# Kernel tuning notes

Hardware: AMD Instinct MI355X
Metric: run time of the kernel (lower is better)

The kernel has to match this reference:

```python
import jax, jax.numpy as jnp
import numpy as np

N_NODES = 100000
N_EDGES = 1600000
F_IN = 128
F_OUT = 64


def setup_inputs() -> dict:
    key = jax.random.key(0)
    kx, kw, kv, ks, kd = jax.random.split(key, 5)
    x = jax.random.normal(kx, (N_NODES, F_IN), dtype=jnp.float32)
    # xavier_uniform init for weight [in, out]
    limit = float(np.sqrt(6.0 / (F_IN + F_OUT)))
    weight = jax.random.uniform(kw, (F_IN, F_OUT), dtype=jnp.float32,
                                minval=-limit, maxval=limit)
    edge_val = jax.random.uniform(kv, (N_EDGES,), dtype=jnp.float32)
    edge_src = jax.random.randint(ks, (N_EDGES,), 0, N_NODES, dtype=jnp.int64)
    edge_dst = jax.random.randint(kd, (N_EDGES,), 0, N_NODES, dtype=jnp.int64)
    return {"x": x, "weight": weight, "edge_val": edge_val,
            "edge_src": edge_src, "edge_dst": edge_dst}


def reference(x, weight, edge_val, edge_src, edge_dst):
    # dropout p = 0.0 -> identity
    support = x @ weight                                  # [N, F_OUT] dense GEMM
    # spmm: out[dst] += val * support[src]  (adj row = dst, col = src)
    messages = support[edge_src] * edge_val[:, None]       # [E, F_OUT] gather
    out = jax.ops.segment_sum(messages, edge_dst,
                              num_segments=x.shape[0])     # [N, F_OUT] scatter-add
    return jax.nn.relu(out)
```

## Files before the change

### kernel.cpp

```cpp
#include <hip/hip_runtime.h>

#define F_IN 128
#define F_OUT 64
#define ROWS_PER_BLOCK 64
#define XSTRIDE 33

#define NPB 128
#define NPB_SHIFT 7
#define BCAP 800
#define ECAP 2560
#define TILE 8192
#define BSTH 1024
#define TMAX 256

__device__ inline unsigned short f2bf(float f) {
    const unsigned u = __float_as_uint(f);
    return (unsigned short)((u + 0x7FFFu + ((u >> 16) & 1u)) >> 16);
}

__global__ __launch_bounds__(512) void gemm_kernel(const float* __restrict__ x,
                                                   const float* __restrict__ w,
                                                   unsigned short* __restrict__ support,
                                                   int n_nodes) {
    __shared__ float4 w_lds[F_IN * F_OUT / 4];
    __shared__ float4 x_lds[ROWS_PER_BLOCK * XSTRIDE];

    const int tid = threadIdx.x;

    {
        const float4* w4 = (const float4*)w;
        #pragma unroll
        for (int i = tid; i < F_IN * F_OUT / 4; i += 512) w_lds[i] = w4[i];
    }

    const int row0 = blockIdx.x * ROWS_PER_BLOCK;
    {
        const float4* x4 = (const float4*)x;
        #pragma unroll
        for (int i = tid; i < ROWS_PER_BLOCK * (F_IN / 4); i += 512) {
            const int r  = i >> 5;
            const int k4 = i & 31;
            const int row = row0 + r;
            float4 v = make_float4(0.f, 0.f, 0.f, 0.f);
            if (row < n_nodes) v = x4[(size_t)row * (F_IN / 4) + k4];
            x_lds[r * XSTRIDE + k4] = v;
        }
    }
    __syncthreads();

    const int tf = tid & 15;
    const int tr = tid >> 4;
    const float* xs = (const float*)x_lds;

    float acc[2][4] = {};
    #pragma unroll 4
    for (int k = 0; k < F_IN; ++k) {
        const float4 wv = w_lds[k * 16 + tf];
        const float x0 = xs[tr * (XSTRIDE * 4) + k];
        const float x1 = xs[(tr + 32) * (XSTRIDE * 4) + k];
        acc[0][0] += x0 * wv.x; acc[0][1] += x0 * wv.y; acc[0][2] += x0 * wv.z; acc[0][3] += x0 * wv.w;
        acc[1][0] += x1 * wv.x; acc[1][1] += x1 * wv.y; acc[1][2] += x1 * wv.z; acc[1][3] += x1 * wv.w;
    }

    #pragma unroll
    for (int i = 0; i < 2; ++i) {
        const int row = row0 + tr + 32 * i;
        if (row < n_nodes) {
            ushort4 o;
            o.x = f2bf(acc[i][0]); o.y = f2bf(acc[i][1]);
            o.z = f2bf(acc[i][2]); o.w = f2bf(acc[i][3]);
            *(ushort4*)&support[(size_t)row * F_OUT + 4 * tf] = o;
        }
    }
}

__global__ __launch_bounds__(BSTH) void bscatter_kernel(const float* __restrict__ edge_val,
                                                        const int* __restrict__ edge_src,
                                                        const int* __restrict__ edge_dst,
                                                        int* __restrict__ toff,
                                                        int2* __restrict__ sorted,
                                                        int n_edges, int nb) {
    __shared__ int2 ebuf[TILE];
    __shared__ unsigned short bkt[TILE];
    __shared__ unsigned short order[TILE];
    __shared__ int h[BCAP];
    __shared__ int lcur[BCAP];
    __shared__ int wsum[16];
    __shared__ int woff_s[16];

    const int tid = threadIdx.x;
    const int te  = blockIdx.x * TILE;
    const int cnt = min(TILE, n_edges - te);

    for (int i = tid; i < BCAP; i += BSTH) h[i] = 0;
    __syncthreads();

    const int cnt4 = cnt >> 2;
    const int4*   s4 = (const int4*)(edge_src + te);
    const int4*   d4 = (const int4*)(edge_dst + te);
    const float4* v4 = (const float4*)(edge_val + te);
    for (int t = tid; t < cnt4; t += BSTH) {
        const int4   s = s4[t];
        const int4   d = d4[t];
        const float4 v = v4[t];
        const int i = t << 2;
        int b;
        b = d.x >> NPB_SHIFT; bkt[i + 0] = (unsigned short)b; atomicAdd(&h[b], 1);
        ebuf[i + 0] = make_int2(s.x | ((d.x & (NPB - 1)) << 20), __float_as_int(v.x));
        b = d.y >> NPB_SHIFT; bkt[i + 1] = (unsigned short)b; atomicAdd(&h[b], 1);
        ebuf[i + 1] = make_int2(s.y | ((d.y & (NPB - 1)) << 20), __float_as_int(v.y));
        b = d.z >> NPB_SHIFT; bkt[i + 2] = (unsigned short)b; atomicAdd(&h[b], 1);
        ebuf[i + 2] = make_int2(s.z | ((d.z & (NPB - 1)) << 20), __float_as_int(v.z));
        b = d.w >> NPB_SHIFT; bkt[i + 3] = (unsigned short)b; atomicAdd(&h[b], 1);
        ebuf[i + 3] = make_int2(s.w | ((d.w & (NPB - 1)) << 20), __float_as_int(v.w));
    }
    for (int e = (cnt4 << 2) + tid; e < cnt; e += BSTH) {
        const int dd = edge_dst[te + e];
        const int b = dd >> NPB_SHIFT;
        bkt[e] = (unsigned short)b;
        atomicAdd(&h[b], 1);
        ebuf[e] = make_int2(edge_src[te + e] | ((dd & (NPB - 1)) << 20),
                            __float_as_int(edge_val[te + e]));
    }
    __syncthreads();

    const int v = (tid < nb) ? h[tid] : 0;
    int s = v;
    #pragma unroll
    for (int off = 1; off < 64; off <<= 1) {
        const int t = __shfl_up(s, off, 64);
        if ((tid & 63) >= off) s += t;
    }
    const int wave = tid >> 6;
    if ((tid & 63) == 63) wsum[wave] = s;
    __syncthreads();
    if (tid < 16) {
        const int ws = wsum[tid];
        int sc = ws;
        #pragma unroll
        for (int off = 1; off < 16; off <<= 1) {
            const int t = __shfl_up(sc, off, 64);
            if (tid >= off) sc += t;
        }
        woff_s[tid] = sc - ws;
    }
    __syncthreads();

    int* trow = toff + (size_t)blockIdx.x * (nb + 1);
    if (tid < nb) {
        const int start = s + woff_s[wave] - v;
        lcur[tid] = start;
        trow[tid] = start;
    }
    if (tid == 0) trow[nb] = cnt;
    __syncthreads();

    for (int i = tid; i < cnt; i += BSTH) {
        const int r = atomicAdd(&lcur[bkt[i]], 1);
        order[r] = (unsigned short)i;
    }
    __syncthreads();
    for (int k = tid; k < cnt; k += BSTH)
        sorted[(size_t)te + k] = ebuf[order[k]];
}

__global__ __launch_bounds__(512) void baccum_kernel(const unsigned short* __restrict__ support,
                                                     const int2* __restrict__ sorted,
                                                     const int* __restrict__ toff,
                                                     float* __restrict__ out,
                                                     int n_nodes, int T, int nb) {
    __shared__ int2 ebuf[ECAP];
    __shared__ int2 ebuf2[ECAP];
    __shared__ int tstart[TMAX];
    __shared__ int toffb[TMAX];
    __shared__ int wsum3[4];
    __shared__ int total_s;
    __shared__ int hist[NPB];
    __shared__ int node_off[NPB + 1];
    __shared__ int cursor[NPB];
    __shared__ int wsum2[2];

    const int tid = threadIdx.x;
    const int b = blockIdx.x;

    int mycnt = 0, myoff = 0;
    if (tid < TMAX) {
        if (tid < T) {
            const int s0 = toff[(size_t)tid * (nb + 1) + b];
            const int e0 = toff[(size_t)tid * (nb + 1) + b + 1];
            toffb[tid] = s0;
            mycnt = e0 - s0;
        }
        int s = mycnt;
        #pragma unroll
        for (int off = 1; off < 64; off <<= 1) {
            const int t = __shfl_up(s, off, 64);
            if ((tid & 63) >= off) s += t;
        }
        if ((tid & 63) == 63) wsum3[tid >> 6] = s;
        myoff = s - mycnt;
    }
    __syncthreads();
    if (tid < TMAX && tid < T) {
        int add = 0;
        const int wv = tid >> 6;
        for (int q = 0; q < wv; ++q) add += wsum3[q];
        tstart[tid] = myoff + add;
    }
    if (tid == 0) total_s = wsum3[0] + wsum3[1] + wsum3[2] + wsum3[3];
    __syncthreads();
    const int total = total_s;

    const int g16 = tid >> 4;
    const int f4  = tid & 15;
    const uint2* sup = (const uint2*)support;

    float4 acc[4];
    #pragma unroll
    for (int j = 0; j < 4; ++j) acc[j] = make_float4(0.f, 0.f, 0.f, 0.f);

    for (int cb = 0; cb < total; cb += ECAP) {
        const int cnt = min(ECAP, total - cb);

        __syncthreads();
        if (tid < NPB) hist[tid] = 0;
        __syncthreads();

        for (int i = tid; i < cnt; i += 512) {
            const int g = cb + i;
            int lo = 0, hi = T - 1;
            while (lo < hi) {
                const int mid = (lo + hi + 1) >> 1;
                if (tstart[mid] <= g) lo = mid; else hi = mid - 1;
            }
            const int2 ev = sorted[(size_t)lo * TILE + toffb[lo] + (g - tstart[lo])];
            ebuf[i] = ev;
            atomicAdd(&hist[((unsigned)ev.x) >> 20], 1);
        }
        __syncthreads();

        {
            int v = 0;
            if (tid < NPB) v = hist[tid];
            int s = v;
            if (tid < NPB) {
                #pragma unroll
                for (int off = 1; off < 64; off <<= 1) {
                    const int t = __shfl_up(s, off, 64);
                    if ((tid & 63) >= off) s += t;
                }
                if ((tid & 63) == 63) wsum2[tid >> 6] = s;
            }
            __syncthreads();
            if (tid < NPB) {
                const int incl = s + ((tid >= 64) ? wsum2[0] : 0);
                node_off[tid + 1] = incl;
                cursor[tid] = incl - v;
                if (tid == 0) node_off[0] = 0;
            }
        }
        __syncthreads();

        for (int i = tid; i < cnt; i += 512) {
            const int2 ev = ebuf[i];
            const int r = atomicAdd(&cursor[((unsigned)ev.x) >> 20], 1);
            ebuf2[r] = ev;
        }
        __syncthreads();

        #pragma unroll
        for (int j = 0; j < 4; ++j) {
            const int nl = g16 + 32 * j;
            int k = node_off[nl];
            const int ke = node_off[nl + 1];
            float4 a = acc[j];
            while (k + 8 <= ke) {
                int2 e[8];
                uint2 s[8];
                #pragma unroll
                for (int u = 0; u < 8; ++u) e[u] = ebuf2[k + u];
                #pragma unroll
                for (int u = 0; u < 8; ++u)
                    s[u] = sup[(size_t)(e[u].x & 0xFFFFF) * 16 + f4];
                #pragma unroll
                for (int u = 0; u < 8; ++u) {
                    const float v = __int_as_float(e[u].y);
                    a.x += v * __uint_as_float(s[u].x << 16);
                    a.y += v * __uint_as_float(s[u].x & 0xFFFF0000u);
                    a.z += v * __uint_as_float(s[u].y << 16);
                    a.w += v * __uint_as_float(s[u].y & 0xFFFF0000u);
                }
                k += 8;
            }
            for (; k < ke; ++k) {
                const int2 e0 = ebuf2[k];
                const uint2 s0 = sup[(size_t)(e0.x & 0xFFFFF) * 16 + f4];
                const float v0 = __int_as_float(e0.y);
                a.x += v0 * __uint_as_float(s0.x << 16);
                a.y += v0 * __uint_as_float(s0.x & 0xFFFF0000u);
                a.z += v0 * __uint_as_float(s0.y << 16);
                a.w += v0 * __uint_as_float(s0.y & 0xFFFF0000u);
            }
            acc[j] = a;
        }
    }

    const int base = b << NPB_SHIFT;
    #pragma unroll
    for (int j = 0; j < 4; ++j) {
        const int node = base + g16 + 32 * j;
        if (node < n_nodes) {
            float4 v = acc[j];
            v.x = fmaxf(v.x, 0.f); v.y = fmaxf(v.y, 0.f);
            v.z = fmaxf(v.z, 0.f); v.w = fmaxf(v.w, 0.f);
            ((float4*)out)[(size_t)node * 16 + f4] = v;
        }
    }
}

__global__ __launch_bounds__(256) void scatter_kernel(const unsigned short* __restrict__ support,
                                                      const float* __restrict__ edge_val,
                                                      const int* __restrict__ edge_src,
                                                      const int* __restrict__ edge_dst,
                                                      float* __restrict__ out,
                                                      int n_edges) {
    const long gid = (long)blockIdx.x * blockDim.x + threadIdx.x;
    const int e = (int)(gid >> 4);
    if (e >= n_edges) return;
    const int q = (int)(gid & 15);
    const int src   = edge_src[e];
    const int dst   = edge_dst[e];
    const float val = edge_val[e];
    const uint2 s = ((const uint2*)support)[(size_t)src * 16 + q];
    float* o = &out[(size_t)dst * F_OUT + q * 4];
    atomicAdd(o + 0, val * __uint_as_float(s.x << 16));
    atomicAdd(o + 1, val * __uint_as_float(s.x & 0xFFFF0000u));
    atomicAdd(o + 2, val * __uint_as_float(s.y << 16));
    atomicAdd(o + 3, val * __uint_as_float(s.y & 0xFFFF0000u));
}

__global__ __launch_bounds__(256) void relu_kernel(float* __restrict__ out, int n4) {
    const int i = blockIdx.x * blockDim.x + threadIdx.x;
    if (i < n4) {
        float4 v = ((float4*)out)[i];
        v.x = fmaxf(v.x, 0.f); v.y = fmaxf(v.y, 0.f);
        v.z = fmaxf(v.z, 0.f); v.w = fmaxf(v.w, 0.f);
        ((float4*)out)[i] = v;
    }
}

extern "C" void kernel_launch(void* const* d_in, const int* in_sizes, int n_in,
                              void* d_out, int out_size, void* d_ws, size_t ws_size,
                              hipStream_t stream) {
    const float* x        = (const float*)d_in[0];
    const float* w        = (const float*)d_in[1];
    const float* edge_val = (const float*)d_in[2];
    const int*   edge_src = (const int*)d_in[3];
    const int*   edge_dst = (const int*)d_in[4];
    float* out = (float*)d_out;

    const int n_nodes = in_sizes[0] / F_IN;
    const int n_edges = in_sizes[2];
    const int nb = (n_nodes + NPB - 1) >> NPB_SHIFT;
    const int T  = (n_edges + TILE - 1) / TILE;

    char* p = (char*)d_ws;
    unsigned short* support = (unsigned short*)p;
    p += (size_t)n_nodes * F_OUT * sizeof(unsigned short);
    p = (char*)(((size_t)p + 15) & ~(size_t)15);
    int2* sorted = (int2*)p;  p += (size_t)T * TILE * sizeof(int2);
    int*  toff   = (int*)p;   p += (size_t)T * (nb + 1) * sizeof(int);
    const size_t ws_needed = (size_t)(p - (char*)d_ws);

    const int gemm_blocks = (n_nodes + ROWS_PER_BLOCK - 1) / ROWS_PER_BLOCK;
    gemm_kernel<<<gemm_blocks, 512, 0, stream>>>(x, w, support, n_nodes);

    const bool ok = (ws_size >= ws_needed) && (nb <= BCAP) && (n_nodes < (1 << 20))
                    && (T <= TMAX);
    if (ok) {
        bscatter_kernel<<<T, BSTH, 0, stream>>>(edge_val, edge_src, edge_dst,
                                                toff, sorted, n_edges, nb);
        baccum_kernel<<<nb, 512, 0, stream>>>(support, sorted, toff, out,
                                              n_nodes, T, nb);
    } else {
        hipMemsetAsync(d_out, 0, (size_t)out_size * sizeof(float), stream);
        const long st = (long)n_edges * 16;
        scatter_kernel<<<(int)((st + 255) / 256), 256, 0, stream>>>(
            support, edge_val, edge_src, edge_dst, out, n_edges);
        const int n4o = out_size / 4;
        relu_kernel<<<(n4o + 255) / 256, 256, 0, stream>>>(out, n4o);
    }
}
```

Measured before the change: 181.6 us.

## Fuse GEMM and edge bucket scatter into one launch with shared LDS union

```diff
diff --git a/kernel.cpp b/kernel.cpp
--- a/kernel.cpp
+++ b/kernel.cpp
@@ -18,113 +18,103 @@
     return (unsigned short)((u + 0x7FFFu + ((u >> 16) & 1u)) >> 16);
 }
 
-__global__ __launch_bounds__(512) void gemm_kernel(const float* __restrict__ x,
-                                                   const float* __restrict__ w,
-                                                   unsigned short* __restrict__ support,
-                                                   int n_nodes) {
-    __shared__ float4 w_lds[F_IN * F_OUT / 4];
-    __shared__ float4 x_lds[ROWS_PER_BLOCK * XSTRIDE];
-
+struct GemmSh {
+    float4 w[F_IN * F_OUT / 4];
+    float4 xt[ROWS_PER_BLOCK * XSTRIDE];
+};
+struct ScatSh {
+    int2 ebuf2[TILE];
+    int  h[BCAP];
+    int  lcur[BCAP];
+    int  wsum[16];
+    int  woff[16];
+};
+union FusedSh { GemmSh g; ScatSh s; };
+
+__global__ __launch_bounds__(BSTH) void fused_kernel(const float* __restrict__ x,
+                                                     const float* __restrict__ w,
+                                                     unsigned short* __restrict__ support,
+                                                     int n_nodes,
+                                                     const float* __restrict__ edge_val,
+                                                     const int* __restrict__ edge_src,
+                                                     const int* __restrict__ edge_dst,
+                                                     int* __restrict__ toff,
+                                                     int2* __restrict__ sorted,
+                                                     int n_edges, int nb, int T) {
+    __shared__ FusedSh u;
     const int tid = threadIdx.x;
 
-    {
-        const float4* w4 = (const float4*)w;
-        #pragma unroll
-        for (int i = tid; i < F_IN * F_OUT / 4; i += 512) w_lds[i] = w4[i];
-    }
-
-    const int row0 = blockIdx.x * ROWS_PER_BLOCK;
-    {
-        const float4* x4 = (const float4*)x;
-        #pragma unroll
-        for (int i = tid; i < ROWS_PER_BLOCK * (F_IN / 4); i += 512) {
-            const int r  = i >> 5;
-            const int k4 = i & 31;
-            const int row = row0 + r;
-            float4 v = make_float4(0.f, 0.f, 0.f, 0.f);
-            if (row < n_nodes) v = x4[(size_t)row * (F_IN / 4) + k4];
-            x_lds[r * XSTRIDE + k4] = v;
-        }
-    }
-    __syncthreads();
-
-    const int tf = tid & 15;
-    const int tr = tid >> 4;
-    const float* xs = (const float*)x_lds;
-
-    float acc[2][4] = {};
-    #pragma unroll 4
-    for (int k = 0; k < F_IN; ++k) {
-        const float4 wv = w_lds[k * 16 + tf];
-        const float x0 = xs[tr * (XSTRIDE * 4) + k];
-        const float x1 = xs[(tr + 32) * (XSTRIDE * 4) + k];
-        acc[0][0] += x0 * wv.x; acc[0][1] += x0 * wv.y; acc[0][2] += x0 * wv.z; acc[0][3] += x0 * wv.w;
-        acc[1][0] += x1 * wv.x; acc[1][1] += x1 * wv.y; acc[1][2] += x1 * wv.z; acc[1][3] += x1 * wv.w;
-    }
-
-    #pragma unroll
-    for (int i = 0; i < 2; ++i) {
-        const int row = row0 + tr + 32 * i;
+    if ((int)blockIdx.x >= T) {
+        const int row0 = (blockIdx.x - T) * ROWS_PER_BLOCK;
+
+        {
+            const float4* w4 = (const float4*)w;
+            #pragma unroll
+            for (int i = tid; i < F_IN * F_OUT / 4; i += BSTH) u.g.w[i] = w4[i];
+        }
+        {
+            const float4* x4 = (const float4*)x;
+            #pragma unroll
+            for (int i = tid; i < ROWS_PER_BLOCK * (F_IN / 4); i += BSTH) {
+                const int r  = i >> 5;
+                const int k4 = i & 31;
+                const int row = row0 + r;
+                float4 v = make_float4(0.f, 0.f, 0.f, 0.f);
+                if (row < n_nodes) v = x4[(size_t)row * (F_IN / 4) + k4];
+                u.g.xt[r * XSTRIDE + k4] = v;
+            }
+        }
+        __syncthreads();
+
+        const int tf = tid & 15;
+        const int tr = tid >> 4;
+        const float* xs = (const float*)u.g.xt;
+
+        float a0 = 0.f, a1 = 0.f, a2 = 0.f, a3 = 0.f;
+        #pragma unroll 4
+        for (int k = 0; k < F_IN; ++k) {
+            const float4 wv = u.g.w[k * 16 + tf];
+            const float xv = xs[tr * (XSTRIDE * 4) + k];
+            a0 += xv * wv.x; a1 += xv * wv.y; a2 += xv * wv.z; a3 += xv * wv.w;
+        }
+        const int row = row0 + tr;
         if (row < n_nodes) {
             ushort4 o;
-            o.x = f2bf(acc[i][0]); o.y = f2bf(acc[i][1]);
-            o.z = f2bf(acc[i][2]); o.w = f2bf(acc[i][3]);
+            o.x = f2bf(a0); o.y = f2bf(a1); o.z = f2bf(a2); o.w = f2bf(a3);
             *(ushort4*)&support[(size_t)row * F_OUT + 4 * tf] = o;
         }
-    }
-}
-
-__global__ __launch_bounds__(BSTH) void bscatter_kernel(const float* __restrict__ edge_val,
-                                                        const int* __restrict__ edge_src,
-                                                        const int* __restrict__ edge_dst,
-                                                        int* __restrict__ toff,
-                                                        int2* __restrict__ sorted,
-                                                        int n_edges, int nb) {
-    __shared__ int2 ebuf[TILE];
-    __shared__ unsigned short bkt[TILE];
-    __shared__ unsigned short order[TILE];
-    __shared__ int h[BCAP];
-    __shared__ int lcur[BCAP];
-    __shared__ int wsum[16];
-    __shared__ int woff_s[16];
-
-    const int tid = threadIdx.x;
+        return;
+    }
+
     const int te  = blockIdx.x * TILE;
     const int cnt = min(TILE, n_edges - te);
 
-    for (int i = tid; i < BCAP; i += BSTH) h[i] = 0;
+    for (int i = tid; i < BCAP; i += BSTH) u.s.h[i] = 0;
     __syncthreads();
 
     const int cnt4 = cnt >> 2;
     const int4*   s4 = (const int4*)(edge_src + te);
     const int4*   d4 = (const int4*)(edge_dst + te);
     const float4* v4 = (const float4*)(edge_val + te);
-    for (int t = tid; t < cnt4; t += BSTH) {
-        const int4   s = s4[t];
-        const int4   d = d4[t];
-        const float4 v = v4[t];
-        const int i = t << 2;
-        int b;
-        b = d.x >> NPB_SHIFT; bkt[i + 0] = (unsigned short)b; atomicAdd(&h[b], 1);
-        ebuf[i + 0] = make_int2(s.x | ((d.x & (NPB - 1)) << 20), __float_as_int(v.x));
-        b = d.y >> NPB_SHIFT; bkt[i + 1] = (unsigned short)b; atomicAdd(&h[b], 1);
-        ebuf[i + 1] = make_int2(s.y | ((d.y & (NPB - 1)) << 20), __float_as_int(v.y));
-        b = d.z >> NPB_SHIFT; bkt[i + 2] = (unsigned short)b; atomicAdd(&h[b], 1);
-        ebuf[i + 2] = make_int2(s.z | ((d.z & (NPB - 1)) << 20), __float_as_int(v.z));
-        b = d.w >> NPB_SHIFT; bkt[i + 3] = (unsigned short)b; atomicAdd(&h[b], 1);
-        ebuf[i + 3] = make_int2(s.w | ((d.w & (NPB - 1)) << 20), __float_as_int(v.w));
-    }
-    for (int e = (cnt4 << 2) + tid; e < cnt; e += BSTH) {
-        const int dd = edge_dst[te + e];
-        const int b = dd >> NPB_SHIFT;
-        bkt[e] = (unsigned short)b;
-        atomicAdd(&h[b], 1);
-        ebuf[e] = make_int2(edge_src[te + e] | ((dd & (NPB - 1)) << 20),
-                            __float_as_int(edge_val[te + e]));
-    }
-    __syncthreads();
-
-    const int v = (tid < nb) ? h[tid] : 0;
+    int4 rs[2], rd[2]; float4 rv[2];
+    #pragma unroll
+    for (int it = 0; it < 2; ++it) {
+        const int t = tid + it * BSTH;
+        if (t < cnt4) {
+            rs[it] = s4[t]; rd[it] = d4[t]; rv[it] = v4[t];
+            atomicAdd(&u.s.h[rd[it].x >> NPB_SHIFT], 1);
+            atomicAdd(&u.s.h[rd[it].y >> NPB_SHIFT], 1);
+            atomicAdd(&u.s.h[rd[it].z >> NPB_SHIFT], 1);
+            atomicAdd(&u.s.h[rd[it].w >> NPB_SHIFT], 1);
+        }
+    }
+    if (tid == 0) {
+        for (int e = cnt4 << 2; e < cnt; ++e)
+            atomicAdd(&u.s.h[edge_dst[te + e] >> NPB_SHIFT], 1);
+    }
+    __syncthreads();
+
+    const int v = (tid < nb) ? u.s.h[tid] : 0;
     int s = v;
     #pragma unroll
     for (int off = 1; off < 64; off <<= 1) {
@@ -132,36 +122,57 @@
         if ((tid & 63) >= off) s += t;
     }
     const int wave = tid >> 6;
-    if ((tid & 63) == 63) wsum[wave] = s;
+    if ((tid & 63) == 63) u.s.wsum[wave] = s;
     __syncthreads();
     if (tid < 16) {
-        const int ws = wsum[tid];
+        const int ws = u.s.wsum[tid];
         int sc = ws;
         #pragma unroll
         for (int off = 1; off < 16; off <<= 1) {
             const int t = __shfl_up(sc, off, 64);
             if (tid >= off) sc += t;
         }
-        woff_s[tid] = sc - ws;
+        u.s.woff[tid] = sc - ws;
     }
     __syncthreads();
 
     int* trow = toff + (size_t)blockIdx.x * (nb + 1);
     if (tid < nb) {
-        const int start = s + woff_s[wave] - v;
-        lcur[tid] = start;
+        const int start = s + u.s.woff[wave] - v;
+        u.s.lcur[tid] = start;
         trow[tid] = start;
     }
     if (tid == 0) trow[nb] = cnt;
     __syncthreads();
 
-    for (int i = tid; i < cnt; i += BSTH) {
-        const int r = atomicAdd(&lcur[bkt[i]], 1);
-        order[r] = (unsigned short)i;
-    }
-    __syncthreads();
+    #pragma unroll
+    for (int it = 0; it < 2; ++it) {
+        const int t = tid + it * BSTH;
+        if (t < cnt4) {
+            int b, r;
+            b = rd[it].x >> NPB_SHIFT; r = atomicAdd(&u.s.lcur[b], 1);
+            u.s.ebuf2[r] = make_int2(rs[it].x | ((rd[it].x & (NPB - 1)) << 20), __float_as_int(rv[it].x));
+            b = rd[it].y >> NPB_SHIFT; r = atomicAdd(&u.s.lcur[b], 1);
+            u.s.ebuf2[r] = make_int2(rs[it].y | ((rd[it].y & (NPB - 1)) << 20), __float_as_int(rv[it].y));
+            b = rd[it].z >> NPB_SHIFT; r = atomicAdd(&u.s.lcur[b], 1);
+            u.s.ebuf2[r] = make_int2(rs[it].z | ((rd[it].z & (NPB - 1)) << 20), __float_as_int(rv[it].z));
+            b = rd[it].w >> NPB_SHIFT; r = atomicAdd(&u.s.lcur[b], 1);
+            u.s.ebuf2[r] = make_int2(rs[it].w | ((rd[it].w & (NPB - 1)) << 20), __float_as_int(rv[it].w));
+        }
+    }
+    if (tid == 0) {
+        for (int e = cnt4 << 2; e < cnt; ++e) {
+            const int dd = edge_dst[te + e];
+            const int b = dd >> NPB_SHIFT;
+            const int r = atomicAdd(&u.s.lcur[b], 1);
+            u.s.ebuf2[r] = make_int2(edge_src[te + e] | ((dd & (NPB - 1)) << 20),
+                                     __float_as_int(edge_val[te + e]));
+        }
+    }
+    __syncthreads();
+
     for (int k = tid; k < cnt; k += BSTH)
-        sorted[(size_t)te + k] = ebuf[order[k]];
+        sorted[(size_t)te + k] = u.s.ebuf2[k];
 }
 
 __global__ __launch_bounds__(512) void baccum_kernel(const unsigned short* __restrict__ support,
@@ -278,17 +289,17 @@
                 int2 e[8];
                 uint2 s[8];
                 #pragma unroll
-                for (int u = 0; u < 8; ++u) e[u] = ebuf2[k + u];
+                for (int u2 = 0; u2 < 8; ++u2) e[u2] = ebuf2[k + u2];
                 #pragma unroll
-                for (int u = 0; u < 8; ++u)
-                    s[u] = sup[(size_t)(e[u].x & 0xFFFFF) * 16 + f4];
+                for (int u2 = 0; u2 < 8; ++u2)
+                    s[u2] = sup[(size_t)(e[u2].x & 0xFFFFF) * 16 + f4];
                 #pragma unroll
-                for (int u = 0; u < 8; ++u) {
-                    const float v = __int_as_float(e[u].y);
-                    a.x += v * __uint_as_float(s[u].x << 16);
-                    a.y += v * __uint_as_float(s[u].x & 0xFFFF0000u);
-                    a.z += v * __uint_as_float(s[u].y << 16);
-                    a.w += v * __uint_as_float(s[u].y & 0xFFFF0000u);
+                for (int u2 = 0; u2 < 8; ++u2) {
+                    const float v = __int_as_float(e[u2].y);
+                    a.x += v * __uint_as_float(s[u2].x << 16);
+                    a.y += v * __uint_as_float(s[u2].x & 0xFFFF0000u);
+                    a.z += v * __uint_as_float(s[u2].y << 16);
+                    a.w += v * __uint_as_float(s[u2].y & 0xFFFF0000u);
                 }
                 k += 8;
             }
@@ -363,6 +374,7 @@
     const int n_edges = in_sizes[2];
     const int nb = (n_nodes + NPB - 1) >> NPB_SHIFT;
     const int T  = (n_edges + TILE - 1) / TILE;
+    const int G  = (n_nodes + ROWS_PER_BLOCK - 1) / ROWS_PER_BLOCK;
 
     char* p = (char*)d_ws;
     unsigned short* support = (unsigned short*)p;
@@ -372,17 +384,18 @@
     int*  toff   = (int*)p;   p += (size_t)T * (nb + 1) * sizeof(int);
     const size_t ws_needed = (size_t)(p - (char*)d_ws);
 
-    const int gemm_blocks = (n_nodes + ROWS_PER_BLOCK - 1) / ROWS_PER_BLOCK;
-    gemm_kernel<<<gemm_blocks, 512, 0, stream>>>(x, w, support, n_nodes);
-
     const bool ok = (ws_size >= ws_needed) && (nb <= BCAP) && (n_nodes < (1 << 20))
                     && (T <= TMAX);
     if (ok) {
-        bscatter_kernel<<<T, BSTH, 0, stream>>>(edge_val, edge_src, edge_dst,
-                                                toff, sorted, n_edges, nb);
+        fused_kernel<<<T + G, BSTH, 0, stream>>>(x, w, support, n_nodes,
+                                                 edge_val, edge_src, edge_dst,
+                                                 toff, sorted, n_edges, nb, T);
         baccum_kernel<<<nb, 512, 0, stream>>>(support, sorted, toff, out,
                                               n_nodes, T, nb);
     } else {
+        fused_kernel<<<G, BSTH, 0, stream>>>(x, w, support, n_nodes,
+                                             edge_val, edge_src, edge_dst,
+                                             nullptr, nullptr, n_edges, nb, 0);
         hipMemsetAsync(d_out, 0, (size_t)out_size * sizeof(float), stream);
         const long st = (long)n_edges * 16;
         scatter_kernel<<<(int)((st + 255) / 256), 256, 0, stream>>>(
```

After: 179.6 us. No clear change (-1.1%).
